# Kernel tuning notes

Measured on AMD Instinct MI355X. Metric: run time of the kernel, lower is better.

The kernel has to match this reference:

```python
import jax, jax.numpy as jnp
import numpy as np

N_NODES = 50000
N_EDGES = 800000
D_IN, D_HID, D_OUT = 128, 128, 64


def _gcn_conv(x, row, col, W, b, num_nodes):
    # Linear (no bias in lin; bias added after aggregation)
    h = x @ W  # [N, d_out]
    # degree over destination (col), includes self-loops
    deg = jax.ops.segment_sum(jnp.ones_like(col, dtype=h.dtype), col, num_segments=num_nodes)
    dis = jnp.where(deg > 0, deg ** -0.5, 0.0)  # deg^{-1/2}, inf -> 0
    norm = dis[row] * dis[col]  # [E+N]
    msg = h[row] * norm[:, None]  # gather + scale
    out = jax.ops.segment_sum(msg, col, num_segments=num_nodes)  # scatter-add
    return out + b


def setup_inputs() -> dict:
    key = jax.random.key(0)
    k1, k2, k3, k4 = jax.random.split(key, 4)
    x = jax.random.normal(k1, (N_NODES, D_IN), dtype=jnp.float32)
    edge_index = jax.random.randint(k2, (2, N_EDGES), 0, N_NODES, dtype=jnp.int32)
    # glorot-like init for linear weights
    W1 = jax.random.normal(k3, (D_IN, D_HID), dtype=jnp.float32) * (2.0 / (D_IN + D_HID)) ** 0.5
    W2 = jax.random.normal(k4, (D_HID, D_OUT), dtype=jnp.float32) * (2.0 / (D_HID + D_OUT)) ** 0.5
    b1 = jnp.zeros((D_HID,), dtype=jnp.float32)
    b2 = jnp.zeros((D_OUT,), dtype=jnp.float32)
    return {"x": x, "edge_index": edge_index, "W1": W1, "b1": b1, "W2": W2, "b2": b2}


def reference(x, edge_index, W1, b1, W2, b2):
    n = x.shape[0]
    # add self-loops
    loops = jnp.arange(n, dtype=edge_index.dtype)
    row = jnp.concatenate([edge_index[0], loops])
    col = jnp.concatenate([edge_index[1], loops])
    h = _gcn_conv(x, row, col, W1, b1, n)
    h = jax.nn.relu(h)  # dropout is identity in eval mode
    out = _gcn_conv(h, row, col, W2, b2, n)
    return out
```

## Files before the change

### kernel.cpp

```cpp
#include <hip/hip_runtime.h>

#define BSH 7
#define BMSK 127
#define NB 391
#define ROWSH 13
#define RCH 7
#define SEG (NB * RCH)
#define NBLK 256
#define BINCAP 3072

typedef __attribute__((ext_vector_type(8))) short short8;
typedef __attribute__((ext_vector_type(4))) float f32x4;
typedef __attribute__((ext_vector_type(4))) unsigned int u32x4;

static inline size_t alignup(size_t x) { return (x + 255) & ~(size_t)255; }

__device__ __forceinline__ unsigned short f2bf(float f) {
    unsigned int u = __float_as_uint(f);
    u = (u + 0x7fffu + ((u >> 16) & 1u)) >> 16;
    return (unsigned short)u;
}

__global__ __launch_bounds__(256) void k_hist(const int* __restrict__ colp,
                                              const int* __restrict__ rowp, int nE,
                                              unsigned* __restrict__ counts,
                                              const float* __restrict__ W1,
                                              const float* __restrict__ W2,
                                              unsigned short* __restrict__ Wt1,
                                              unsigned short* __restrict__ Wt2) {
    int blk = blockIdx.x;
    if (blk >= NBLK) {
        int i = (blk - NBLK) * 256 + threadIdx.x;
        if (i < 128 * 128) { int k = i >> 7, c = i & 127; Wt1[(size_t)c * 128 + k] = f2bf(W1[i]); }
        if (i < 128 * 64)  { int k = i >> 6, c = i & 63;  Wt2[(size_t)c * 128 + k] = f2bf(W2[i]); }
        return;
    }
    __shared__ unsigned h[SEG];
    for (int i = threadIdx.x; i < SEG; i += 256) h[i] = 0;
    __syncthreads();
    int chunk = (nE + NBLK - 1) / NBLK;
    int e0 = blk * chunk, e1 = min(nE, e0 + chunk);
    for (int e = e0 + (int)threadIdx.x; e < e1; e += 256) {
        int c = colp[e], r = rowp[e];
        atomicAdd(&h[(c >> BSH) * RCH + (r >> ROWSH)], 1u);
    }
    __syncthreads();
    for (int i = threadIdx.x; i < SEG; i += 256) counts[(size_t)i * NBLK + blk] = h[i];
}

__global__ __launch_bounds__(NBLK) void k_scanA(unsigned* __restrict__ counts,
                                                unsigned* __restrict__ segtot) {
    int seg = blockIdx.x, t = threadIdx.x;
    __shared__ unsigned ps[NBLK];
    unsigned s = counts[(size_t)seg * NBLK + t];
    ps[t] = s;
    __syncthreads();
    for (int d = 1; d < NBLK; d <<= 1) {
        unsigned v = (t >= d) ? ps[t - d] : 0u;
        __syncthreads();
        ps[t] += v;
        __syncthreads();
    }
    counts[(size_t)seg * NBLK + t] = ps[t] - s;
    if (t == NBLK - 1) segtot[seg] = ps[NBLK - 1];
}

__global__ __launch_bounds__(256) void k_scatgemm(const int* __restrict__ colp,
                                                  const int* __restrict__ rowp, int nE,
                                                  const unsigned* __restrict__ counts,
                                                  const unsigned* __restrict__ segtot,
                                                  unsigned* __restrict__ pairs,
                                                  unsigned* __restrict__ edgebase,
                                                  const float* __restrict__ x,
                                                  const unsigned short* __restrict__ Wt1,
                                                  unsigned short* __restrict__ hs1, int M) {
    if ((int)blockIdx.x < NBLK) {
        __shared__ unsigned sb[SEG];
        __shared__ unsigned ts[256];
        int t = threadIdx.x, blk = blockIdx.x;
        for (int i = t; i < SEG; i += 256) sb[i] = segtot[i];
        __syncthreads();
        const int CH = (SEG + 255) / 256;
        unsigned s = 0;
#pragma unroll
        for (int j = 0; j < CH; ++j) {
            int idx = t * CH + j;
            if (idx < SEG) s += sb[idx];
        }
        ts[t] = s;
        __syncthreads();
        for (int d = 1; d < 256; d <<= 1) {
            unsigned v = (t >= d) ? ts[t - d] : 0u;
            __syncthreads();
            ts[t] += v;
            __syncthreads();
        }
        unsigned run = ts[t] - s;
        unsigned loc[CH > 0 ? CH : 1];
#pragma unroll
        for (int j = 0; j < CH; ++j) {
            int idx = t * CH + j;
            if (idx < SEG) { unsigned v = sb[idx]; loc[j] = run; run += v; }
        }
        __syncthreads();
#pragma unroll
        for (int j = 0; j < CH; ++j) {
            int idx = t * CH + j;
            if (idx < SEG) sb[idx] = loc[j];
        }
        __syncthreads();
        if (blk == 0) {
            for (int b = t; b < NB; b += 256) edgebase[b] = sb[b * RCH];
            if (t == 0) edgebase[NB] = (unsigned)nE;
        }
        for (int i = t; i < SEG; i += 256) sb[i] += counts[(size_t)i * NBLK + blk];
        __syncthreads();
        int chunk = (nE + NBLK - 1) / NBLK;
        int e0 = blk * chunk, e1 = min(nE, e0 + chunk);
        for (int e = e0 + (int)t; e < e1; e += 256) {
            int c = colp[e], r = rowp[e];
            unsigned pos = atomicAdd(&sb[(c >> BSH) * RCH + (r >> ROWSH)], 1u);
            pairs[pos] = ((unsigned)r << BSH) | (unsigned)(c & BMSK);
        }
        return;
    }
    const int NT = 8;
    const int bid = blockIdx.x - NBLK;
    const int lane = threadIdx.x & 63;
    const int wave = threadIdx.x >> 6;
    const int m0 = bid * 64 + wave * 16;
    const int lrow = lane & 15;
    const int lk = lane >> 4;
    int arow = m0 + lrow;
    if (arow >= M) arow = M - 1;

    f32x4 acc[NT];
#pragma unroll
    for (int t = 0; t < NT; ++t) acc[t] = (f32x4){0.f, 0.f, 0.f, 0.f};

#pragma unroll
    for (int k0 = 0; k0 < 4; ++k0) {
        const int kb = k0 * 32 + lk * 8;
        const float* ap = &x[(size_t)arow * 128 + kb];
        f32x4 v0 = __builtin_nontemporal_load((const f32x4*)ap);
        f32x4 v1 = __builtin_nontemporal_load((const f32x4*)(ap + 4));
        short8 afrag;
#pragma unroll
        for (int q = 0; q < 4; ++q) {
            afrag[q] = (short)f2bf(v0[q]);
            afrag[4 + q] = (short)f2bf(v1[q]);
        }
#pragma unroll
        for (int t = 0; t < NT; ++t) {
            const int bcol = t * 16 + lrow;
            short8 bfrag = *(const short8*)&Wt1[(size_t)bcol * 128 + kb];
            acc[t] = __builtin_amdgcn_mfma_f32_16x16x32_bf16(afrag, bfrag, acc[t], 0, 0, 0);
        }
    }
#pragma unroll
    for (int i = 0; i < 4; ++i) {
        int row = m0 + lk * 4 + i;
        if (row < M) {
#pragma unroll
            for (int t = 0; t < NT; ++t)
                hs1[(size_t)row * 128 + t * 16 + lrow] = f2bf(acc[t][i]);
        }
    }
}

__global__ __launch_bounds__(256) void k_binbuild(const unsigned* __restrict__ pairs,
                                                  const unsigned* __restrict__ edgebase,
                                                  unsigned* __restrict__ csr,
                                                  unsigned* __restrict__ off,
                                                  float* __restrict__ dis, int n) {
    __shared__ unsigned lp[BINCAP];
    __shared__ unsigned lr[BINCAP];
    __shared__ unsigned hist[128];
    __shared__ unsigned scn[128];
    int b = blockIdx.x, t = threadIdx.x;
    unsigned e0 = edgebase[b], e1 = edgebase[b + 1];
    unsigned ec = e1 - e0;
    if (ec > BINCAP) ec = BINCAP;
    if (t < 128) hist[t] = 0;
    __syncthreads();
    for (unsigned i = t; i < ec; i += 256) {
        unsigned v = pairs[e0 + i];
        lp[i] = v;
        atomicAdd(&hist[v & BMSK], 1u);
    }
    __syncthreads();
    unsigned hv = (t < 128) ? hist[t] : 0u;
    if (t < 128) scn[t] = hv;
    __syncthreads();
    for (int d = 1; d < 128; d <<= 1) {
        unsigned v = (t < 128 && t >= d) ? scn[t - d] : 0u;
        __syncthreads();
        if (t < 128) scn[t] += v;
        __syncthreads();
    }
    unsigned ex = (t < 128) ? scn[t] - hv : 0u;
    int node = (b << BSH) + t;
    if (t < 128 && node < n) {
        off[node] = e0 + ex;
        dis[node] = rsqrtf((float)(hv + 1));
    }
    if (b == NB - 1 && t == 0) off[n] = e1;
    __syncthreads();
    if (t < 128) scn[t] = ex;
    __syncthreads();
    for (unsigned i = t; i < ec; i += 256) {
        unsigned v = lp[i];
        unsigned pos = atomicAdd(&scn[v & BMSK], 1u);
        lr[pos] = v >> BSH;
    }
    __syncthreads();
    for (unsigned i = t; i < ec; i += 256) csr[e0 + i] = lr[i];
}

__device__ __forceinline__ void acc8s(float a[8], u32x4 u, float d) {
    a[0] = fmaf(__uint_as_float(u[0] << 16), d, a[0]);
    a[1] = fmaf(__uint_as_float(u[0] & 0xffff0000u), d, a[1]);
    a[2] = fmaf(__uint_as_float(u[1] << 16), d, a[2]);
    a[3] = fmaf(__uint_as_float(u[1] & 0xffff0000u), d, a[3]);
    a[4] = fmaf(__uint_as_float(u[2] << 16), d, a[4]);
    a[5] = fmaf(__uint_as_float(u[2] & 0xffff0000u), d, a[5]);
    a[6] = fmaf(__uint_as_float(u[3] << 16), d, a[6]);
    a[7] = fmaf(__uint_as_float(u[3] & 0xffff0000u), d, a[7]);
}

__device__ __forceinline__ void acc8(float a[8], u32x4 u) {
    a[0] += __uint_as_float(u[0] << 16);
    a[1] += __uint_as_float(u[0] & 0xffff0000u);
    a[2] += __uint_as_float(u[1] << 16);
    a[3] += __uint_as_float(u[1] & 0xffff0000u);
    a[4] += __uint_as_float(u[2] << 16);
    a[5] += __uint_as_float(u[2] & 0xffff0000u);
    a[6] += __uint_as_float(u[3] << 16);
    a[7] += __uint_as_float(u[3] & 0xffff0000u);
}

__global__ __launch_bounds__(256) void k_fuse2(const unsigned short* __restrict__ hs1,
                                               const unsigned* __restrict__ csr,
                                               const unsigned* __restrict__ off,
                                               const float* __restrict__ dis,
                                               const float* __restrict__ b1,
                                               const unsigned short* __restrict__ Wt2,
                                               unsigned short* __restrict__ hs2, int n) {
    __shared__ unsigned short st[16 * 136];
    const int tid = threadIdx.x;
    int vloc = tid >> 4;
    int c = tid & 15;
    int v = blockIdx.x * 16 + vloc;
    if (v >= n) v = n - 1;

    const u32x4* h4 = (const u32x4*)hs1;
    size_t base = (size_t)v * 16 + c;
    unsigned s = off[v], e = off[v + 1];
    float dv = dis[v];

    float a[8];
#pragma unroll
    for (int j = 0; j < 8; ++j) a[j] = 0.f;
    acc8s(a, h4[base], dv);

    unsigned i = s;
    for (; i + 8 <= e; i += 8) {
        unsigned r[8];
        float d[8];
        u32x4 m[8];
#pragma unroll
        for (int j = 0; j < 8; ++j) r[j] = csr[i + j];
#pragma unroll
        for (int j = 0; j < 8; ++j) d[j] = dis[r[j]];
#pragma unroll
        for (int j = 0; j < 8; ++j) m[j] = h4[(size_t)r[j] * 16 + c];
#pragma unroll
        for (int j = 0; j < 8; ++j) acc8s(a, m[j], d[j]);
    }
    if (i + 4 <= e) {
        unsigned r0 = csr[i], r1 = csr[i + 1], r2 = csr[i + 2], r3 = csr[i + 3];
        float d0 = dis[r0], d1 = dis[r1], d2 = dis[r2], d3 = dis[r3];
        u32x4 m0 = h4[(size_t)r0 * 16 + c];
        u32x4 m1 = h4[(size_t)r1 * 16 + c];
        u32x4 m2 = h4[(size_t)r2 * 16 + c];
        u32x4 m3 = h4[(size_t)r3 * 16 + c];
        acc8s(a, m0, d0); acc8s(a, m1, d1); acc8s(a, m2, d2); acc8s(a, m3, d3);
        i += 4;
    }
    for (; i < e; ++i) {
        unsigned r = csr[i];
        acc8s(a, h4[(size_t)r * 16 + c], dis[r]);
    }

    u32x4 pk;
#pragma unroll
    for (int q = 0; q < 4; ++q) {
        float lo = fmaxf(a[2 * q] * dv + b1[c * 8 + 2 * q], 0.f);
        float hi = fmaxf(a[2 * q + 1] * dv + b1[c * 8 + 2 * q + 1], 0.f);
        pk[q] = (unsigned)f2bf(lo) | ((unsigned)f2bf(hi) << 16);
    }
    *(u32x4*)&st[vloc * 136 + c * 8] = pk;
    __syncthreads();

    const int lane = tid & 63;
    const int wave = tid >> 6;
    const int lrow = lane & 15;
    const int lk = lane >> 4;
    f32x4 acc = (f32x4){0.f, 0.f, 0.f, 0.f};
#pragma unroll
    for (int k0 = 0; k0 < 4; ++k0) {
        const int kb = k0 * 32 + lk * 8;
        short8 afrag = *(const short8*)&st[lrow * 136 + kb];
        const int bcol = wave * 16 + lrow;
        short8 bfrag = *(const short8*)&Wt2[(size_t)bcol * 128 + kb];
        acc = __builtin_amdgcn_mfma_f32_16x16x32_bf16(afrag, bfrag, acc, 0, 0, 0);
    }
#pragma unroll
    for (int i2 = 0; i2 < 4; ++i2) {
        int row = blockIdx.x * 16 + lk * 4 + i2;
        if (row < n) {
            float sc = dis[row];
            hs2[(size_t)row * 64 + wave * 16 + lrow] = f2bf(acc[i2] * sc);
        }
    }
}

__global__ __launch_bounds__(256) void k_gather2(const unsigned short* __restrict__ hs,
                                                 const unsigned* __restrict__ csr,
                                                 const unsigned* __restrict__ off,
                                                 const float* __restrict__ dis,
                                                 const float* __restrict__ bias,
                                                 float* __restrict__ outp, int n) {
    int v = blockIdx.x * 32 + (int)(threadIdx.x >> 3);
    int c = threadIdx.x & 7;
    if (v >= n) return;
    const u32x4* h4 = (const u32x4*)hs;
    size_t base = (size_t)v * 8 + c;

    unsigned s = off[v], e = off[v + 1];
    float dv = dis[v];

    float a[8];
#pragma unroll
    for (int j = 0; j < 8; ++j) a[j] = 0.f;
    acc8(a, h4[base]);

    unsigned i = s;
    for (; i + 8 <= e; i += 8) {
        unsigned r[8];
        u32x4 m[8];
#pragma unroll
        for (int j = 0; j < 8; ++j) r[j] = csr[i + j];
#pragma unroll
        for (int j = 0; j < 8; ++j) m[j] = h4[(size_t)r[j] * 8 + c];
#pragma unroll
        for (int j = 0; j < 8; ++j) acc8(a, m[j]);
    }
    if (i + 4 <= e) {
        unsigned r0 = csr[i], r1 = csr[i + 1], r2 = csr[i + 2], r3 = csr[i + 3];
        u32x4 m0 = h4[(size_t)r0 * 8 + c];
        u32x4 m1 = h4[(size_t)r1 * 8 + c];
        u32x4 m2 = h4[(size_t)r2 * 8 + c];
        u32x4 m3 = h4[(size_t)r3 * 8 + c];
        acc8(a, m0); acc8(a, m1); acc8(a, m2); acc8(a, m3);
        i += 4;
    }
    for (; i < e; ++i) acc8(a, h4[(size_t)csr[i] * 8 + c]);

    float rr[8];
#pragma unroll
    for (int j = 0; j < 8; ++j) rr[j] = a[j] * dv + bias[c * 8 + j];
    f32x4 lov = {rr[0], rr[1], rr[2], rr[3]};
    f32x4 hiv = {rr[4], rr[5], rr[6], rr[7]};
    __builtin_nontemporal_store(lov, (f32x4*)&outp[(size_t)v * 64 + c * 8]);
    __builtin_nontemporal_store(hiv, (f32x4*)&outp[(size_t)v * 64 + c * 8 + 4]);
}

extern "C" void kernel_launch(void* const* d_in, const int* in_sizes, int n_in,
                              void* d_out, int out_size, void* d_ws, size_t ws_size,
                              hipStream_t stream) {
    const float* x  = (const float*)d_in[0];
    const int*   ei = (const int*)d_in[1];
    const float* W1 = (const float*)d_in[2];
    const float* b1 = (const float*)d_in[3];
    const float* W2 = (const float*)d_in[4];
    const float* b2 = (const float*)d_in[5];

    const int Din = 128;
    const int Nn = in_sizes[0] / Din;
    const int E  = in_sizes[1] / 2;
    const int* rowp = ei;
    const int* colp = ei + E;

    char* ws = (char*)d_ws;
    size_t off_ = 0;
    unsigned*       counts   = (unsigned*)(ws + off_);       off_ = alignup(off_ + (size_t)SEG * NBLK * 4);
    unsigned*       segtot   = (unsigned*)(ws + off_);       off_ = alignup(off_ + (size_t)SEG * 4);
    unsigned*       edgebase = (unsigned*)(ws + off_);       off_ = alignup(off_ + (size_t)(NB + 1) * 4);
    unsigned*       pairs    = (unsigned*)(ws + off_);       off_ = alignup(off_ + (size_t)E * 4);
    unsigned*       csr      = (unsigned*)(ws + off_);       off_ = alignup(off_ + (size_t)E * 4);
    unsigned*       offv     = (unsigned*)(ws + off_);       off_ = alignup(off_ + (size_t)(Nn + 1) * 4);
    float*          dis      = (float*)(ws + off_);          off_ = alignup(off_ + (size_t)Nn * 4);
    unsigned short* Wt1      = (unsigned short*)(ws + off_); off_ = alignup(off_ + 128 * 128 * 2);
    unsigned short* Wt2      = (unsigned short*)(ws + off_); off_ = alignup(off_ + 128 * 64 * 2);
    unsigned short* hs1      = (unsigned short*)(ws + off_); off_ = alignup(off_ + (size_t)Nn * 128 * 2);
    unsigned short* hs2      = (unsigned short*)(ws + off_); off_ = alignup(off_ + (size_t)Nn * 64 * 2);
    float*          outp     = (float*)d_out;

    const int G1 = (Nn + 63) / 64;

    k_hist<<<NBLK + 64, 256, 0, stream>>>(colp, rowp, E, counts, W1, W2, Wt1, Wt2);
    k_scanA<<<SEG, NBLK, 0, stream>>>(counts, segtot);
    k_scatgemm<<<NBLK + G1, 256, 0, stream>>>(colp, rowp, E, counts, segtot,
                                              pairs, edgebase, x, Wt1, hs1, Nn);
    k_binbuild<<<NB, 256, 0, stream>>>(pairs, edgebase, csr, offv, dis, Nn);

    k_fuse2<<<(Nn + 15) / 16, 256, 0, stream>>>(hs1, csr, offv, dis, b1, Wt2, hs2, Nn);

    k_gather2<<<(Nn + 31) / 32, 256, 0, stream>>>(hs2, csr, offv, dis, b2, outp, Nn);
}
```

Baseline: 120.1 us.

## Move row-chunk sub-sorting into bin build and overlap layer-1 GEMM with histogram

The global counting sort now keys only on destination bin (391 segments) instead of bin×row-chunk, which shrinks the counts array and the scan. The row-chunk ordering is kept by moving it into the per-bin LDS sort in k_binbuild, through a 128×7 key histogram and a block-wide scan. The layer-1 GEMM now runs in the same launch as the histogram instead of with the scatter, and the scatter uses 128 blocks. This adds one kernel launch and a heavier scan in binbuild in exchange for less global atomic and scan work.

```diff
diff --git a/kernel.cpp b/kernel.cpp
--- a/kernel.cpp
+++ b/kernel.cpp
@@ -4,9 +4,8 @@
 #define BMSK 127
 #define NB 391
 #define ROWSH 13
-#define RCH 7
-#define SEG (NB * RCH)
-#define NBLK 256
+#define NCH 7
+#define NBLKS 128
 #define BINCAP 3072
 
 typedef __attribute__((ext_vector_type(8))) short short8;
@@ -21,114 +20,37 @@
     return (unsigned short)u;
 }
 
-__global__ __launch_bounds__(256) void k_hist(const int* __restrict__ colp,
-                                              const int* __restrict__ rowp, int nE,
-                                              unsigned* __restrict__ counts,
-                                              const float* __restrict__ W1,
+__global__ __launch_bounds__(256) void k_prep(const float* __restrict__ W1,
                                               const float* __restrict__ W2,
                                               unsigned short* __restrict__ Wt1,
                                               unsigned short* __restrict__ Wt2) {
-    int blk = blockIdx.x;
-    if (blk >= NBLK) {
-        int i = (blk - NBLK) * 256 + threadIdx.x;
-        if (i < 128 * 128) { int k = i >> 7, c = i & 127; Wt1[(size_t)c * 128 + k] = f2bf(W1[i]); }
-        if (i < 128 * 64)  { int k = i >> 6, c = i & 63;  Wt2[(size_t)c * 128 + k] = f2bf(W2[i]); }
+    int i = blockIdx.x * 256 + threadIdx.x;
+    if (i < 128 * 128) { int k = i >> 7, c = i & 127; Wt1[(size_t)c * 128 + k] = f2bf(W1[i]); }
+    if (i < 128 * 64)  { int k = i >> 6, c = i & 63;  Wt2[(size_t)c * 128 + k] = f2bf(W2[i]); }
+}
+
+__global__ __launch_bounds__(256) void k_front(const float* __restrict__ x,
+                                               const unsigned short* __restrict__ Wt1,
+                                               unsigned short* __restrict__ hs1, int M,
+                                               const int* __restrict__ colp, int nE,
+                                               unsigned* __restrict__ counts, int G1) {
+    if ((int)blockIdx.x >= G1) {
+        int blk = blockIdx.x - G1;
+        __shared__ unsigned h[NB];
+        for (int i = threadIdx.x; i < NB; i += 256) h[i] = 0;
+        __syncthreads();
+        int chunk = (nE + NBLKS - 1) / NBLKS;
+        int e0 = blk * chunk, e1 = min(nE, e0 + chunk);
+        for (int e = e0 + (int)threadIdx.x; e < e1; e += 256)
+            atomicAdd(&h[colp[e] >> BSH], 1u);
+        __syncthreads();
+        for (int i = threadIdx.x; i < NB; i += 256) counts[(size_t)i * NBLKS + blk] = h[i];
         return;
     }
-    __shared__ unsigned h[SEG];
-    for (int i = threadIdx.x; i < SEG; i += 256) h[i] = 0;
-    __syncthreads();
-    int chunk = (nE + NBLK - 1) / NBLK;
-    int e0 = blk * chunk, e1 = min(nE, e0 + chunk);
-    for (int e = e0 + (int)threadIdx.x; e < e1; e += 256) {
-        int c = colp[e], r = rowp[e];
-        atomicAdd(&h[(c >> BSH) * RCH + (r >> ROWSH)], 1u);
-    }
-    __syncthreads();
-    for (int i = threadIdx.x; i < SEG; i += 256) counts[(size_t)i * NBLK + blk] = h[i];
-}
-
-__global__ __launch_bounds__(NBLK) void k_scanA(unsigned* __restrict__ counts,
-                                                unsigned* __restrict__ segtot) {
-    int seg = blockIdx.x, t = threadIdx.x;
-    __shared__ unsigned ps[NBLK];
-    unsigned s = counts[(size_t)seg * NBLK + t];
-    ps[t] = s;
-    __syncthreads();
-    for (int d = 1; d < NBLK; d <<= 1) {
-        unsigned v = (t >= d) ? ps[t - d] : 0u;
-        __syncthreads();
-        ps[t] += v;
-        __syncthreads();
-    }
-    counts[(size_t)seg * NBLK + t] = ps[t] - s;
-    if (t == NBLK - 1) segtot[seg] = ps[NBLK - 1];
-}
-
-__global__ __launch_bounds__(256) void k_scatgemm(const int* __restrict__ colp,
-                                                  const int* __restrict__ rowp, int nE,
-                                                  const unsigned* __restrict__ counts,
-                                                  const unsigned* __restrict__ segtot,
-                                                  unsigned* __restrict__ pairs,
-                                                  unsigned* __restrict__ edgebase,
-                                                  const float* __restrict__ x,
-                                                  const unsigned short* __restrict__ Wt1,
-                                                  unsigned short* __restrict__ hs1, int M) {
-    if ((int)blockIdx.x < NBLK) {
-        __shared__ unsigned sb[SEG];
-        __shared__ unsigned ts[256];
-        int t = threadIdx.x, blk = blockIdx.x;
-        for (int i = t; i < SEG; i += 256) sb[i] = segtot[i];
-        __syncthreads();
-        const int CH = (SEG + 255) / 256;
-        unsigned s = 0;
-#pragma unroll
-        for (int j = 0; j < CH; ++j) {
-            int idx = t * CH + j;
-            if (idx < SEG) s += sb[idx];
-        }
-        ts[t] = s;
-        __syncthreads();
-        for (int d = 1; d < 256; d <<= 1) {
-            unsigned v = (t >= d) ? ts[t - d] : 0u;
-            __syncthreads();
-            ts[t] += v;
-            __syncthreads();
-        }
-        unsigned run = ts[t] - s;
-        unsigned loc[CH > 0 ? CH : 1];
-#pragma unroll
-        for (int j = 0; j < CH; ++j) {
-            int idx = t * CH + j;
-            if (idx < SEG) { unsigned v = sb[idx]; loc[j] = run; run += v; }
-        }
-        __syncthreads();
-#pragma unroll
-        for (int j = 0; j < CH; ++j) {
-            int idx = t * CH + j;
-            if (idx < SEG) sb[idx] = loc[j];
-        }
-        __syncthreads();
-        if (blk == 0) {
-            for (int b = t; b < NB; b += 256) edgebase[b] = sb[b * RCH];
-            if (t == 0) edgebase[NB] = (unsigned)nE;
-        }
-        for (int i = t; i < SEG; i += 256) sb[i] += counts[(size_t)i * NBLK + blk];
-        __syncthreads();
-        int chunk = (nE + NBLK - 1) / NBLK;
-        int e0 = blk * chunk, e1 = min(nE, e0 + chunk);
-        for (int e = e0 + (int)t; e < e1; e += 256) {
-            int c = colp[e], r = rowp[e];
-            unsigned pos = atomicAdd(&sb[(c >> BSH) * RCH + (r >> ROWSH)], 1u);
-            pairs[pos] = ((unsigned)r << BSH) | (unsigned)(c & BMSK);
-        }
-        return;
-    }
     const int NT = 8;
-    const int bid = blockIdx.x - NBLK;
     const int lane = threadIdx.x & 63;
     const int wave = threadIdx.x >> 6;
-    const int m0 = bid * 64 + wave * 16;
+    const int m0 = blockIdx.x * 64 + wave * 16;
     const int lrow = lane & 15;
     const int lk = lane >> 4;
     int arow = m0 + lrow;
@@ -165,6 +87,74 @@
             for (int t = 0; t < NT; ++t)
                 hs1[(size_t)row * 128 + t * 16 + lrow] = f2bf(acc[t][i]);
         }
+    }
+}
+
+__global__ __launch_bounds__(NBLKS) void k_scanA(unsigned* __restrict__ counts,
+                                                 unsigned* __restrict__ bintot) {
+    int bin = blockIdx.x, t = threadIdx.x;
+    __shared__ unsigned ps[NBLKS];
+    unsigned s = counts[(size_t)bin * NBLKS + t];
+    ps[t] = s;
+    __syncthreads();
+    for (int d = 1; d < NBLKS; d <<= 1) {
+        unsigned v = (t >= d) ? ps[t - d] : 0u;
+        __syncthreads();
+        ps[t] += v;
+        __syncthreads();
+    }
+    counts[(size_t)bin * NBLKS + t] = ps[t] - s;
+    if (t == NBLKS - 1) bintot[bin] = ps[NBLKS - 1];
+}
+
+__global__ __launch_bounds__(256) void k_scatter(const int* __restrict__ colp,
+                                                 const int* __restrict__ rowp, int nE,
+                                                 const unsigned* __restrict__ counts,
+                                                 const unsigned* __restrict__ bintot,
+                                                 unsigned* __restrict__ pairs,
+                                                 unsigned* __restrict__ edgebase) {
+    __shared__ unsigned bb[NB];
+    __shared__ unsigned ts[256];
+    int t = threadIdx.x, blk = blockIdx.x;
+    for (int i = t; i < NB; i += 256) bb[i] = bintot[i];
+    __syncthreads();
+    const int CH = (NB + 255) / 256;
+    unsigned s = 0;
+    unsigned own[CH];
+#pragma unroll
+    for (int j = 0; j < CH; ++j) {
+        int idx = t * CH + j;
+        unsigned v = (idx < NB) ? bb[idx] : 0u;
+        own[j] = s; s += v;
+    }
+    ts[t] = s;
+    __syncthreads();
+    for (int d = 1; d < 256; d <<= 1) {
+        unsigned v = (t >= d) ? ts[t - d] : 0u;
+        __syncthreads();
+        ts[t] += v;
+        __syncthreads();
+    }
+    unsigned base = ts[t] - s;
+    __syncthreads();
+#pragma unroll
+    for (int j = 0; j < CH; ++j) {
+        int idx = t * CH + j;
+        if (idx < NB) bb[idx] = base + own[j];
+    }
+    __syncthreads();
+    if (blk == 0) {
+        for (int b = t; b < NB; b += 256) edgebase[b] = bb[b];
+        if (t == 0) edgebase[NB] = (unsigned)nE;
+    }
+    for (int i = t; i < NB; i += 256) bb[i] += counts[(size_t)i * NBLKS + blk];
+    __syncthreads();
+    int chunk = (nE + NBLKS - 1) / NBLKS;
+    int e0 = blk * chunk, e1 = min(nE, e0 + chunk);
+    for (int e = e0 + (int)t; e < e1; e += 256) {
+        int c = colp[e], r = rowp[e];
+        unsigned pos = atomicAdd(&bb[c >> BSH], 1u);
+        pairs[pos] = ((unsigned)r << BSH) | (unsigned)(c & BMSK);
     }
 }
 
@@ -175,42 +165,61 @@
                                                   float* __restrict__ dis, int n) {
     __shared__ unsigned lp[BINCAP];
     __shared__ unsigned lr[BINCAP];
-    __shared__ unsigned hist[128];
-    __shared__ unsigned scn[128];
+    __shared__ unsigned hist[128 * NCH];
+    __shared__ unsigned scn[256];
     int b = blockIdx.x, t = threadIdx.x;
     unsigned e0 = edgebase[b], e1 = edgebase[b + 1];
     unsigned ec = e1 - e0;
     if (ec > BINCAP) ec = BINCAP;
-    if (t < 128) hist[t] = 0;
+    for (int i = t; i < 128 * NCH; i += 256) hist[i] = 0;
     __syncthreads();
     for (unsigned i = t; i < ec; i += 256) {
         unsigned v = pairs[e0 + i];
         lp[i] = v;
-        atomicAdd(&hist[v & BMSK], 1u);
-    }
-    __syncthreads();
-    unsigned hv = (t < 128) ? hist[t] : 0u;
-    if (t < 128) scn[t] = hv;
-    __syncthreads();
-    for (int d = 1; d < 128; d <<= 1) {
-        unsigned v = (t < 128 && t >= d) ? scn[t - d] : 0u;
-        __syncthreads();
-        if (t < 128) scn[t] += v;
-        __syncthreads();
-    }
-    unsigned ex = (t < 128) ? scn[t] - hv : 0u;
-    int node = (b << BSH) + t;
-    if (t < 128 && node < n) {
-        off[node] = e0 + ex;
-        dis[node] = rsqrtf((float)(hv + 1));
+        unsigned key = (v & BMSK) * NCH + ((v >> BSH) >> ROWSH);
+        atomicAdd(&hist[key], 1u);
+    }
+    __syncthreads();
+    const int HCH = 4;
+    unsigned own[HCH];
+    unsigned s = 0;
+#pragma unroll
+    for (int j = 0; j < HCH; ++j) {
+        int idx = t * HCH + j;
+        unsigned v = (idx < 128 * NCH) ? hist[idx] : 0u;
+        own[j] = s; s += v;
+    }
+    scn[t] = s;
+    __syncthreads();
+    for (int d = 1; d < 256; d <<= 1) {
+        unsigned v = (t >= d) ? scn[t - d] : 0u;
+        __syncthreads();
+        scn[t] += v;
+        __syncthreads();
+    }
+    unsigned base = scn[t] - s;
+    __syncthreads();
+#pragma unroll
+    for (int j = 0; j < HCH; ++j) {
+        int idx = t * HCH + j;
+        if (idx < 128 * NCH) hist[idx] = base + own[j];
+    }
+    __syncthreads();
+    if (t < 128) {
+        int node = (b << BSH) + t;
+        if (node < n) {
+            unsigned start = hist[t * NCH];
+            unsigned next = (t == 127) ? ec : hist[(t + 1) * NCH];
+            off[node] = e0 + start;
+            dis[node] = rsqrtf((float)(next - start + 1));
+        }
     }
     if (b == NB - 1 && t == 0) off[n] = e1;
-    __syncthreads();
-    if (t < 128) scn[t] = ex;
     __syncthreads();
     for (unsigned i = t; i < ec; i += 256) {
         unsigned v = lp[i];
-        unsigned pos = atomicAdd(&scn[v & BMSK], 1u);
+        unsigned key = (v & BMSK) * NCH + ((v >> BSH) >> ROWSH);
+        unsigned pos = atomicAdd(&hist[key], 1u);
         lr[pos] = v >> BSH;
     }
     __syncthreads();
@@ -394,8 +403,8 @@
 
     char* ws = (char*)d_ws;
     size_t off_ = 0;
-    unsigned*       counts   = (unsigned*)(ws + off_);       off_ = alignup(off_ + (size_t)SEG * NBLK * 4);
-    unsigned*       segtot   = (unsigned*)(ws + off_);       off_ = alignup(off_ + (size_t)SEG * 4);
+    unsigned*       counts   = (unsigned*)(ws + off_);       off_ = alignup(off_ + (size_t)NB * NBLKS * 4);
+    unsigned*       bintot   = (unsigned*)(ws + off_);       off_ = alignup(off_ + (size_t)NB * 4);
     unsigned*       edgebase = (unsigned*)(ws + off_);       off_ = alignup(off_ + (size_t)(NB + 1) * 4);
     unsigned*       pairs    = (unsigned*)(ws + off_);       off_ = alignup(off_ + (size_t)E * 4);
     unsigned*       csr      = (unsigned*)(ws + off_);       off_ = alignup(off_ + (size_t)E * 4);
@@ -409,10 +418,10 @@
 
     const int G1 = (Nn + 63) / 64;
 
-    k_hist<<<NBLK + 64, 256, 0, stream>>>(colp, rowp, E, counts, W1, W2, Wt1, Wt2);
-    k_scanA<<<SEG, NBLK, 0, stream>>>(counts, segtot);
-    k_scatgemm<<<NBLK + G1, 256, 0, stream>>>(colp, rowp, E, counts, segtot,
-                                              pairs, edgebase, x, Wt1, hs1, Nn);
+    k_prep<<<64, 256, 0, stream>>>(W1, W2, Wt1, Wt2);
+    k_front<<<G1 + NBLKS, 256, 0, stream>>>(x, Wt1, hs1, Nn, colp, E, counts, G1);
+    k_scanA<<<NB, NBLKS, 0, stream>>>(counts, bintot);
+    k_scatter<<<NBLKS, 256, 0, stream>>>(colp, rowp, E, counts, bintot, pairs, edgebase);
     k_binbuild<<<NB, 256, 0, stream>>>(pairs, edgebase, csr, offv, dis, Nn);
 
     k_fuse2<<<(Nn + 15) / 16, 256, 0, stream>>>(hs1, csr, offv, dis, b1, Wt2, hs2, Nn);
```

Measured after the change: 111.5 us. -7.2%, faster.
